# Kernel optimization log

Hardware: AMD Instinct MI355X
Metric: run time of the kernel (lower is better)

The kernel has to match this reference:

```python
import jax, jax.numpy as jnp
import numpy as np

DISTANCE_THRESHOLD = 100.0  # squared-distance threshold (cdist**2 <= thresh)
NO_CODE_ID = -1


def setup_inputs() -> dict:
    key = jax.random.key(0)
    kx, kc = jax.random.split(key)
    x = jax.random.normal(kx, (2, 1024, 64), dtype=jnp.float32)      # [b, s, d] query tokens
    codes = jax.random.normal(kc, (50000, 64), dtype=jnp.float32)    # [n, d] active code bank
    return {"x": x, "codes": codes}


def reference(x, codes):
    # squared euclidean distances, matching torch.cdist(x, codes) ** 2
    x2 = jnp.sum(x * x, axis=-1, keepdims=True)            # [b, s, 1]
    c2 = jnp.sum(codes * codes, axis=-1)                   # [n]
    cross = jnp.einsum('bsd,nd->bsn', x, codes)            # [b, s, n]
    d2 = jnp.maximum(x2 + c2 - 2.0 * cross, 0.0)           # clamp tiny negatives, cdist >= 0

    within = jnp.any(d2 <= DISTANCE_THRESHOLD, axis=-1)    # [b, s]
    nn_ids = jnp.argmin(d2, axis=-1)                       # [b, s]
    return jnp.where(within, nn_ids, NO_CODE_ID)
```

## Files before the change

### kernel.cpp

```cpp
#include <hip/hip_runtime.h>

#define NTOK   2048
#define DIM    64
#define NCODES 50000
#define THRESH 100.0f
#define BIG    3.0e38f
#define MARGIN 4.0f
#define NBLK   391
#define BM32   1564
#define BM32P  1568
#define NCG    64

typedef __attribute__((ext_vector_type(8)))  __bf16 bf16x8;
typedef __attribute__((ext_vector_type(16))) float  float16;

__device__ __forceinline__ unsigned short f2bf(float f) {
    union { float f; unsigned int u; } v; v.f = f;
    unsigned int r = v.u + 0x7FFF + ((v.u >> 16) & 1);
    return (unsigned short)(r >> 16);
}
__device__ __forceinline__ unsigned int pack2(float a, float b) {
    return (unsigned int)f2bf(a) | ((unsigned int)f2bf(b) << 16);
}
__device__ __forceinline__ float max16(const float16& v) {
    float a = fmaxf(v[0], v[1]),   b = fmaxf(v[2], v[3]);
    float c = fmaxf(v[4], v[5]),   d = fmaxf(v[6], v[7]);
    float e = fmaxf(v[8], v[9]),   f = fmaxf(v[10], v[11]);
    float g = fmaxf(v[12], v[13]), h = fmaxf(v[14], v[15]);
    a = fmaxf(a, b); c = fmaxf(c, d); e = fmaxf(e, f); g = fmaxf(g, h);
    return fmaxf(fmaxf(a, c), fmaxf(e, g));
}

__global__ __launch_bounds__(256, 2)
void nn_stageA_kernel(const float* __restrict__ x,
                      const float* __restrict__ codes,
                      float* __restrict__ bm32) {
    __shared__ __bf16 cs[128 * 72];
    __shared__ float  c2s[128];

    const int tid  = threadIdx.x;
    const int w    = tid >> 6;
    const int lane = tid & 63;
    const int l31  = lane & 31;
    const int h    = lane >> 5;
    const int gi   = blockIdx.x;
    const int g0   = 6 * gi + min(gi, 7);
    const int nb   = (gi < 7) ? 7 : 6;
    const int t0   = blockIdx.y * 256;
    const int row_ = tid >> 3;
    const int seg  = tid & 7;

    bf16x8 bfr[4][2];
#pragma unroll
    for (int s = 0; s < 4; ++s)
#pragma unroll
        for (int nj = 0; nj < 2; ++nj) {
            const float4* xp = (const float4*)(x +
                (size_t)(t0 + w * 64 + nj * 32 + l31) * DIM + s * 16 + h * 8);
            float4 a = xp[0], b = xp[1];
            uint4 u;
            u.x = pack2(a.x, a.y); u.y = pack2(a.z, a.w);
            u.z = pack2(b.x, b.y); u.w = pack2(b.z, b.w);
            bfr[s][nj] = *(bf16x8*)&u;
        }

    float4 pra[4], prb[4];
    auto prefetch = [&](int blk) {
        int n0 = blk * 128;
#pragma unroll
        for (int it = 0; it < 4; ++it) {
            int n = n0 + it * 32 + row_;
            if (n < NCODES) {
                const float4* cp = (const float4*)(codes + (size_t)n * DIM + seg * 8);
                pra[it] = cp[0]; prb[it] = cp[1];
            } else {
                pra[it] = make_float4(0.f, 0.f, 0.f, 0.f);
                prb[it] = pra[it];
            }
        }
    };
    prefetch(g0);

    for (int t = 0; t < nb; ++t) {
        const int blk = g0 + t;
        __syncthreads();

#pragma unroll
        for (int it = 0; it < 4; ++it) {
            int row = it * 32 + row_;
            float4 a = pra[it], b = prb[it];
            float s = a.x * a.x;
            s = fmaf(a.y, a.y, s); s = fmaf(a.z, a.z, s); s = fmaf(a.w, a.w, s);
            s = fmaf(b.x, b.x, s); s = fmaf(b.y, b.y, s);
            s = fmaf(b.z, b.z, s); s = fmaf(b.w, b.w, s);
            s += __shfl_xor(s, 1);
            s += __shfl_xor(s, 2);
            s += __shfl_xor(s, 4);
            uint4 u;
            u.x = pack2(a.x, a.y); u.y = pack2(a.z, a.w);
            u.z = pack2(b.x, b.y); u.w = pack2(b.z, b.w);
            *(uint4*)&cs[row * 72 + seg * 8] = u;
            if (seg == 0)
                c2s[row] = (blk * 128 + row < NCODES) ? -0.5f * s : -0.5f * BIG;
        }
        if (t + 1 < nb) prefetch(blk + 1);
        __syncthreads();

        float16 acc[4][2];
#pragma unroll
        for (int mi = 0; mi < 4; ++mi)
#pragma unroll
            for (int g2 = 0; g2 < 4; ++g2) {
                float4 c4 = *(float4*)&c2s[mi * 32 + g2 * 8 + 4 * h];
#pragma unroll
                for (int i = 0; i < 4; ++i) {
                    float iv = ((float*)&c4)[i];
                    acc[mi][0][g2 * 4 + i] = iv;
                    acc[mi][1][g2 * 4 + i] = iv;
                }
            }

#pragma unroll
        for (int s = 0; s < 4; ++s) {
            bf16x8 a[4];
#pragma unroll
            for (int mi = 0; mi < 4; ++mi)
                a[mi] = *(bf16x8*)&cs[(mi * 32 + l31) * 72 + s * 16 + h * 8];
#pragma unroll
            for (int mi = 0; mi < 4; ++mi)
#pragma unroll
                for (int nj = 0; nj < 2; ++nj)
                    acc[mi][nj] = __builtin_amdgcn_mfma_f32_32x32x16_bf16(
                        a[mi], bfr[s][nj], acc[mi][nj], 0, 0, 0);
        }

        float4 o[2];
#pragma unroll
        for (int nj = 0; nj < 2; ++nj)
#pragma unroll
            for (int mi = 0; mi < 4; ++mi) {
                float m = max16(acc[mi][nj]);
                m = fmaxf(m, __shfl_xor(m, 32));
                ((float*)&o[nj])[mi] = -2.0f * m;
            }
        float4 ov = (lane < 32) ? o[0] : o[1];
        int token = t0 + w * 64 + lane;
        *(float4*)&bm32[(size_t)token * BM32P + blk * 4] = ov;
    }
}

__global__ __launch_bounds__(256)
void nn_finalize_kernel(const float* __restrict__ x,
                        const float* __restrict__ codes,
                        const float* __restrict__ bm32,
                        int* __restrict__ out) {
    __shared__ float redf[8];
    __shared__ int   redi[4];
    __shared__ int   queue[BM32];
    __shared__ int   qcount;
    __shared__ float gshare;

    const int tid  = threadIdx.x;
    const int w    = tid >> 6;
    const int lane = tid & 63;
    const int t    = blockIdx.x;
    const float* bm = bm32 + (size_t)t * BM32P;

    if (tid == 0) qcount = 0;

    float v[7];
    float g = BIG;
#pragma unroll
    for (int k = 0; k < 7; ++k) {
        int b = tid + k * 256;
        v[k] = (b < BM32) ? bm[b] : BIG;
        g = fminf(g, v[k]);
    }
#pragma unroll
    for (int m = 1; m < 64; m <<= 1) g = fminf(g, __shfl_xor(g, m));
    if (lane == 0) redf[w] = g;
    __syncthreads();
    if (tid == 0)
        gshare = fminf(fminf(redf[0], redf[1]), fminf(redf[2], redf[3])) + MARGIN;
    __syncthreads();
    const float th = gshare;

#pragma unroll
    for (int k = 0; k < 7; ++k) {
        int b = tid + k * 256;
        if (v[k] <= th) {
            int slot = atomicAdd(&qcount, 1);
            queue[slot] = b;
        }
    }
    __syncthreads();
    const int nq = qcount;

    const int half = lane & 1;
    float4 xh[8];
#pragma unroll
    for (int q = 0; q < 8; ++q)
        xh[q] = *(const float4*)(x + (size_t)t * DIM + half * 32 + q * 4);
    float x2v = 0.f;
#pragma unroll
    for (int q = 0; q < 8; ++q) {
        x2v = fmaf(xh[q].x, xh[q].x, x2v);
        x2v = fmaf(xh[q].y, xh[q].y, x2v);
        x2v = fmaf(xh[q].z, xh[q].z, x2v);
        x2v = fmaf(xh[q].w, xh[q].w, x2v);
    }
    x2v += __shfl_xor(x2v, 1);

    float bv = BIG;
    int   bi = 0x7fffffff;
    for (int e = w; e < nq; e += 4) {
        int blk = queue[e];
        int n = blk * 32 + (lane >> 1);
        if (n < NCODES) {
            const float4* cp = (const float4*)(codes + (size_t)n * DIM + half * 32);
            float d = 0.f, cq = 0.f;
#pragma unroll
            for (int q = 0; q < 8; ++q) {
                float4 c4 = cp[q];
                d  = fmaf(xh[q].x, c4.x, d);
                d  = fmaf(xh[q].y, c4.y, d);
                d  = fmaf(xh[q].z, c4.z, d);
                d  = fmaf(xh[q].w, c4.w, d);
                cq = fmaf(c4.x, c4.x, cq);
                cq = fmaf(c4.y, c4.y, cq);
                cq = fmaf(c4.z, c4.z, cq);
                cq = fmaf(c4.w, c4.w, cq);
            }
            d  += __shfl_xor(d, 1);
            cq += __shfl_xor(cq, 1);
            float d2 = fmaxf(fmaf(-2.f, d, x2v + cq), 0.f);
            if (d2 < bv || (d2 == bv && n < bi)) { bv = d2; bi = n; }
        }
    }
#pragma unroll
    for (int m = 1; m < 64; m <<= 1) {
        float vv = __shfl_xor(bv, m);
        int   ii = __shfl_xor(bi, m);
        if (vv < bv || (vv == bv && ii < bi)) { bv = vv; bi = ii; }
    }
    if (lane == 0) { redf[4 + w] = bv; redi[w] = bi; }
    __syncthreads();
    if (tid == 0) {
        float fb = BIG;
        int   fi = 0x7fffffff;
#pragma unroll
        for (int i = 0; i < 4; ++i) {
            float vv = redf[4 + i];
            int   ii = redi[i];
            if (vv < fb || (vv == fb && ii < fi)) { fb = vv; fi = ii; }
        }
        out[t] = (fb <= THRESH) ? fi : -1;
    }
}

extern "C" void kernel_launch(void* const* d_in, const int* in_sizes, int n_in,
                              void* d_out, int out_size, void* d_ws, size_t ws_size,
                              hipStream_t stream) {
    const float* x     = (const float*)d_in[0];
    const float* codes = (const float*)d_in[1];
    float* bm32 = (float*)d_ws;
    int* out = (int*)d_out;

    nn_stageA_kernel<<<dim3(NCG, 8), 256, 0, stream>>>(x, codes, bm32);
    nn_finalize_kernel<<<NTOK, 256, 0, stream>>>(x, codes, bm32, out);
}
```

Before: 131.3 us.

## Transpose block-max buffer and process 16 tokens per finalize workgroup

Stage A now writes the per-32-code block maxima transposed (block-major, token-minor), so the finalize kernel can read 16 tokens' values with coalesced loads. The finalize kernel handles 16 tokens per workgroup instead of one. It keeps x in shared memory, finds per-token thresholds, and rescans candidate blocks with ballot and a per-candidate wave reduction in place of a shared queue. This cuts the number of finalize workgroups and replaces strided per-token row reads. The cost is scalar, strided stores in stage A, reading bm twice, and a full 64-lane reduction for each candidate.

```diff
diff --git a/kernel.cpp b/kernel.cpp
--- a/kernel.cpp
+++ b/kernel.cpp
@@ -8,8 +8,10 @@
 #define MARGIN 4.0f
 #define NBLK   391
 #define BM32   1564
-#define BM32P  1568
 #define NCG    64
+#define TB     16
+#define NFWG   (NTOK/TB)
+#define NB16   98
 
 typedef __attribute__((ext_vector_type(8)))  __bf16 bf16x8;
 typedef __attribute__((ext_vector_type(16))) float  float16;
@@ -34,7 +36,7 @@
 __global__ __launch_bounds__(256, 2)
 void nn_stageA_kernel(const float* __restrict__ x,
                       const float* __restrict__ codes,
-                      float* __restrict__ bm32) {
+                      float* __restrict__ bmT) {
     __shared__ __bf16 cs[128 * 72];
     __shared__ float  c2s[128];
 
@@ -145,116 +147,126 @@
             }
         float4 ov = (lane < 32) ? o[0] : o[1];
         int token = t0 + w * 64 + lane;
-        *(float4*)&bm32[(size_t)token * BM32P + blk * 4] = ov;
+#pragma unroll
+        for (int mi = 0; mi < 4; ++mi)
+            bmT[(size_t)(blk * 4 + mi) * NTOK + token] = ((float*)&ov)[mi];
     }
 }
 
 __global__ __launch_bounds__(256)
 void nn_finalize_kernel(const float* __restrict__ x,
                         const float* __restrict__ codes,
-                        const float* __restrict__ bm32,
+                        const float* __restrict__ bmT,
                         int* __restrict__ out) {
-    __shared__ float redf[8];
-    __shared__ int   redi[4];
-    __shared__ int   queue[BM32];
-    __shared__ int   qcount;
-    __shared__ float gshare;
+    __shared__ float xs[TB * DIM];
+    __shared__ float x2s[TB];
+    __shared__ float thS[TB];
+    __shared__ float gW[4][TB];
+    __shared__ float bvW[4][TB];
+    __shared__ int   biW[4][TB];
 
     const int tid  = threadIdx.x;
     const int w    = tid >> 6;
     const int lane = tid & 63;
-    const int t    = blockIdx.x;
-    const float* bm = bm32 + (size_t)t * BM32P;
-
-    if (tid == 0) qcount = 0;
-
-    float v[7];
+    const int t0   = blockIdx.x * TB;
+    const int tloc = lane & 15;
+    const int bslt = lane >> 4;
+
+    {
+        int tok = tid >> 4, seg = tid & 15;
+        *(float4*)&xs[tok * DIM + seg * 4] =
+            *(const float4*)(x + (size_t)(t0 + tok) * DIM + seg * 4);
+    }
+    if (tid < 2 * TB) {
+        int tok = tid >> 1, hf = tid & 1;
+        const float4* xp = (const float4*)(x + (size_t)(t0 + tok) * DIM + hf * 32);
+        float s = 0.f;
+#pragma unroll
+        for (int q = 0; q < 8; ++q) {
+            float4 a = xp[q];
+            s = fmaf(a.x, a.x, s); s = fmaf(a.y, a.y, s);
+            s = fmaf(a.z, a.z, s); s = fmaf(a.w, a.w, s);
+        }
+        s += __shfl_xor(s, 1);
+        if (hf == 0) x2s[tok] = s;
+    }
+    if (tid < 64) { bvW[tid >> 4][tid & 15] = BIG; biW[tid >> 4][tid & 15] = 0x7fffffff; }
+
+    const float* bp = bmT + t0 + tloc;
     float g = BIG;
-#pragma unroll
-    for (int k = 0; k < 7; ++k) {
-        int b = tid + k * 256;
-        v[k] = (b < BM32) ? bm[b] : BIG;
-        g = fminf(g, v[k]);
-    }
-#pragma unroll
-    for (int m = 1; m < 64; m <<= 1) g = fminf(g, __shfl_xor(g, m));
-    if (lane == 0) redf[w] = g;
+#pragma unroll 7
+    for (int it = 0; it < NB16; ++it) {
+        int b = it * 16 + (w << 2) + bslt;
+        float v = (b < BM32) ? bp[(size_t)b * NTOK] : BIG;
+        g = fminf(g, v);
+    }
+    g = fminf(g, __shfl_xor(g, 16));
+    g = fminf(g, __shfl_xor(g, 32));
+    if (lane < 16) gW[w][tloc] = g;
     __syncthreads();
-    if (tid == 0)
-        gshare = fminf(fminf(redf[0], redf[1]), fminf(redf[2], redf[3])) + MARGIN;
+    if (tid < TB)
+        thS[tid] = fminf(fminf(gW[0][tid], gW[1][tid]),
+                         fminf(gW[2][tid], gW[3][tid])) + MARGIN;
     __syncthreads();
-    const float th = gshare;
-
-#pragma unroll
-    for (int k = 0; k < 7; ++k) {
-        int b = tid + k * 256;
-        if (v[k] <= th) {
-            int slot = atomicAdd(&qcount, 1);
-            queue[slot] = b;
-        }
-    }
-    __syncthreads();
-    const int nq = qcount;
 
     const int half = lane & 1;
-    float4 xh[8];
-#pragma unroll
-    for (int q = 0; q < 8; ++q)
-        xh[q] = *(const float4*)(x + (size_t)t * DIM + half * 32 + q * 4);
-    float x2v = 0.f;
-#pragma unroll
-    for (int q = 0; q < 8; ++q) {
-        x2v = fmaf(xh[q].x, xh[q].x, x2v);
-        x2v = fmaf(xh[q].y, xh[q].y, x2v);
-        x2v = fmaf(xh[q].z, xh[q].z, x2v);
-        x2v = fmaf(xh[q].w, xh[q].w, x2v);
-    }
-    x2v += __shfl_xor(x2v, 1);
-
-    float bv = BIG;
-    int   bi = 0x7fffffff;
-    for (int e = w; e < nq; e += 4) {
-        int blk = queue[e];
-        int n = blk * 32 + (lane >> 1);
-        if (n < NCODES) {
-            const float4* cp = (const float4*)(codes + (size_t)n * DIM + half * 32);
+    for (int it = 0; it < NB16; ++it) {
+        int b = it * 16 + (w << 2) + bslt;
+        float v = (b < BM32) ? bp[(size_t)b * NTOK] : BIG;
+        unsigned long long mask = __ballot(v <= thS[tloc]);
+        while (mask) {
+            int l = __ffsll(mask) - 1;
+            mask &= mask - 1;
+            int bc = __shfl(b, l);
+            int tc = l & 15;
+            int n  = bc * 32 + (lane >> 1);
+            bool valid = (n < NCODES);
             float d = 0.f, cq = 0.f;
-#pragma unroll
-            for (int q = 0; q < 8; ++q) {
-                float4 c4 = cp[q];
-                d  = fmaf(xh[q].x, c4.x, d);
-                d  = fmaf(xh[q].y, c4.y, d);
-                d  = fmaf(xh[q].z, c4.z, d);
-                d  = fmaf(xh[q].w, c4.w, d);
-                cq = fmaf(c4.x, c4.x, cq);
-                cq = fmaf(c4.y, c4.y, cq);
-                cq = fmaf(c4.z, c4.z, cq);
-                cq = fmaf(c4.w, c4.w, cq);
+            if (valid) {
+                const float4* cp = (const float4*)(codes + (size_t)n * DIM + half * 32);
+                const float4* xp = (const float4*)&xs[tc * DIM + half * 32];
+#pragma unroll
+                for (int q = 0; q < 8; ++q) {
+                    float4 c4 = cp[q];
+                    float4 a  = xp[q];
+                    d  = fmaf(a.x, c4.x, d);
+                    d  = fmaf(a.y, c4.y, d);
+                    d  = fmaf(a.z, c4.z, d);
+                    d  = fmaf(a.w, c4.w, d);
+                    cq = fmaf(c4.x, c4.x, cq);
+                    cq = fmaf(c4.y, c4.y, cq);
+                    cq = fmaf(c4.z, c4.z, cq);
+                    cq = fmaf(c4.w, c4.w, cq);
+                }
             }
             d  += __shfl_xor(d, 1);
             cq += __shfl_xor(cq, 1);
-            float d2 = fmaxf(fmaf(-2.f, d, x2v + cq), 0.f);
-            if (d2 < bv || (d2 == bv && n < bi)) { bv = d2; bi = n; }
-        }
-    }
-#pragma unroll
-    for (int m = 1; m < 64; m <<= 1) {
-        float vv = __shfl_xor(bv, m);
-        int   ii = __shfl_xor(bi, m);
-        if (vv < bv || (vv == bv && ii < bi)) { bv = vv; bi = ii; }
-    }
-    if (lane == 0) { redf[4 + w] = bv; redi[w] = bi; }
+            float d2 = valid ? fmaxf(fmaf(-2.f, d, x2s[tc] + cq), 0.f) : BIG;
+            int   ni = valid ? n : 0x7fffffff;
+#pragma unroll
+            for (int m = 1; m < 64; m <<= 1) {
+                float vv = __shfl_xor(d2, m);
+                int   ii = __shfl_xor(ni, m);
+                if (vv < d2 || (vv == d2 && ii < ni)) { d2 = vv; ni = ii; }
+            }
+            if (lane == 0) {
+                if (d2 < bvW[w][tc] || (d2 == bvW[w][tc] && ni < biW[w][tc])) {
+                    bvW[w][tc] = d2; biW[w][tc] = ni;
+                }
+            }
+        }
+    }
     __syncthreads();
-    if (tid == 0) {
+    if (tid < TB) {
         float fb = BIG;
         int   fi = 0x7fffffff;
 #pragma unroll
         for (int i = 0; i < 4; ++i) {
-            float vv = redf[4 + i];
-            int   ii = redi[i];
+            float vv = bvW[i][tid];
+            int   ii = biW[i][tid];
             if (vv < fb || (vv == fb && ii < fi)) { fb = vv; fi = ii; }
         }
-        out[t] = (fb <= THRESH) ? fi : -1;
+        out[t0 + tid] = (fb <= THRESH) ? fi : -1;
     }
 }
 
@@ -263,9 +275,9 @@
                               hipStream_t stream) {
     const float* x     = (const float*)d_in[0];
     const float* codes = (const float*)d_in[1];
-    float* bm32 = (float*)d_ws;
+    float* bmT = (float*)d_ws;
     int* out = (int*)d_out;
 
-    nn_stageA_kernel<<<dim3(NCG, 8), 256, 0, stream>>>(x, codes, bm32);
-    nn_finalize_kernel<<<NTOK, 256, 0, stream>>>(x, codes, bm32, out);
-}
+    nn_stageA_kernel<<<dim3(NCG, 8), 256, 0, stream>>>(x, codes, bmT);
+    nn_finalize_kernel<<<NFWG, 256, 0, stream>>>(x, codes, bmT, out);
+}
```

After: 184.1 us. 40.3% more time.

## Transpose block-min buffer to block-major layout and double stage-A grid

Applied to the files above, without the earlier changes.

Stores per-block partial maxima in a block-major float4 layout so stage-A writes from a wave are fully coalesced, and finalize reads each block's float4 with a strided gather. Doubles the number of code-group blocks (each handling 3-4 tiles instead of 6-7) and raises launch-bounds occupancy to 4 blocks per CU. Finalize remaps block IDs so consecutive blocks read adjacent tokens, improving cache-line sharing for the strided reads. It risks register spills under the tighter occupancy bound and adds more per-block x fragment loads.

```diff
diff --git a/kernel.cpp b/kernel.cpp
--- a/kernel.cpp
+++ b/kernel.cpp
@@ -8,8 +8,7 @@
 #define MARGIN 4.0f
 #define NBLK   391
 #define BM32   1564
-#define BM32P  1568
-#define NCG    64
+#define NCG    128
 
 typedef __attribute__((ext_vector_type(8)))  __bf16 bf16x8;
 typedef __attribute__((ext_vector_type(16))) float  float16;
@@ -31,10 +30,10 @@
     return fmaxf(fmaxf(a, c), fmaxf(e, g));
 }
 
-__global__ __launch_bounds__(256, 2)
+__global__ __launch_bounds__(256, 4)
 void nn_stageA_kernel(const float* __restrict__ x,
                       const float* __restrict__ codes,
-                      float* __restrict__ bm32) {
+                      float4* __restrict__ bmB) {
     __shared__ __bf16 cs[128 * 72];
     __shared__ float  c2s[128];
 
@@ -44,8 +43,8 @@
     const int l31  = lane & 31;
     const int h    = lane >> 5;
     const int gi   = blockIdx.x;
-    const int g0   = 6 * gi + min(gi, 7);
-    const int nb   = (gi < 7) ? 7 : 6;
+    const int g0   = 3 * gi + min(gi, 7);
+    const int nb   = (gi < 7) ? 4 : 3;
     const int t0   = blockIdx.y * 256;
     const int row_ = tid >> 3;
     const int seg  = tid & 7;
@@ -145,14 +144,14 @@
             }
         float4 ov = (lane < 32) ? o[0] : o[1];
         int token = t0 + w * 64 + lane;
-        *(float4*)&bm32[(size_t)token * BM32P + blk * 4] = ov;
+        bmB[(size_t)blk * NTOK + token] = ov;
     }
 }
 
 __global__ __launch_bounds__(256)
 void nn_finalize_kernel(const float* __restrict__ x,
                         const float* __restrict__ codes,
-                        const float* __restrict__ bm32,
+                        const float4* __restrict__ bmB,
                         int* __restrict__ out) {
     __shared__ float redf[8];
     __shared__ int   redi[4];
@@ -163,19 +162,19 @@
     const int tid  = threadIdx.x;
     const int w    = tid >> 6;
     const int lane = tid & 63;
-    const int t    = blockIdx.x;
-    const float* bm = bm32 + (size_t)t * BM32P;
+    const int bid  = blockIdx.x;
+    const int t    = (bid & 7) * 256 + (bid >> 3);
+    const float4* bp = bmB + t;
 
     if (tid == 0) qcount = 0;
 
-    float v[7];
-    float g = BIG;
-#pragma unroll
-    for (int k = 0; k < 7; ++k) {
-        int b = tid + k * 256;
-        v[k] = (b < BM32) ? bm[b] : BIG;
-        g = fminf(g, v[k]);
-    }
+    float4 v0 = bp[(size_t)tid * NTOK];
+    const bool has1 = (tid + 256) < NBLK;
+    float4 v1 = has1 ? bp[(size_t)(tid + 256) * NTOK]
+                     : make_float4(BIG, BIG, BIG, BIG);
+
+    float g = fminf(fminf(fminf(v0.x, v0.y), fminf(v0.z, v0.w)),
+                    fminf(fminf(v1.x, v1.y), fminf(v1.z, v1.w)));
 #pragma unroll
     for (int m = 1; m < 64; m <<= 1) g = fminf(g, __shfl_xor(g, m));
     if (lane == 0) redf[w] = g;
@@ -185,12 +184,16 @@
     __syncthreads();
     const float th = gshare;
 
-#pragma unroll
-    for (int k = 0; k < 7; ++k) {
-        int b = tid + k * 256;
-        if (v[k] <= th) {
-            int slot = atomicAdd(&qcount, 1);
-            queue[slot] = b;
+    {
+        const float* f0 = (const float*)&v0;
+#pragma unroll
+        for (int c = 0; c < 4; ++c)
+            if (f0[c] <= th) queue[atomicAdd(&qcount, 1)] = tid * 4 + c;
+        if (has1) {
+            const float* f1 = (const float*)&v1;
+#pragma unroll
+            for (int c = 0; c < 4; ++c)
+                if (f1[c] <= th) queue[atomicAdd(&qcount, 1)] = (tid + 256) * 4 + c;
         }
     }
     __syncthreads();
@@ -263,9 +266,9 @@
                               hipStream_t stream) {
     const float* x     = (const float*)d_in[0];
     const float* codes = (const float*)d_in[1];
-    float* bm32 = (float*)d_ws;
+    float4* bmB = (float4*)d_ws;
     int* out = (int*)d_out;
 
-    nn_stageA_kernel<<<dim3(NCG, 8), 256, 0, stream>>>(x, codes, bm32);
-    nn_finalize_kernel<<<NTOK, 256, 0, stream>>>(x, codes, bm32, out);
-}
+    nn_stageA_kernel<<<dim3(NCG, 8), 256, 0, stream>>>(x, codes, bmB);
+    nn_finalize_kernel<<<NTOK, 256, 0, stream>>>(x, codes, bmB, out);
+}
```

Measured after the change: 232.9 us. 1.77x slower.
